# Kernel tuning notes

Hardware: AMD Instinct MI355X
Metric: run time of the kernel (lower is better)

## Reference

```python
import jax, jax.numpy as jnp
import numpy as np

D = 64          # data dimension
K = 16          # latent dimension
N = 65536       # number of samples
P = 2           # max_permutations
BETA = 10.0     # noise precision


def setup_inputs() -> dict:
    key = jax.random.key(0)
    kz, kw, ke, kp = jax.random.split(key, 4)
    W = jax.random.normal(kw, (D, K), jnp.float32)
    Z = jax.random.normal(kz, (N, K), jnp.float32)
    eps = (1.0 / BETA) * jax.random.normal(ke, (N, 1), jnp.float32)
    x = Z @ W.T + eps  # (N, D), matches the repo's generative model
    # one permutation of 0..D-1 per (dim a, permutation p)
    keys = jax.random.split(kp, D * P)
    perms = jax.vmap(lambda k: jax.random.permutation(k, D))(keys)
    perms = perms.reshape(D, P, D).astype(jnp.int32)
    return {"x": x, "W": W, "perms": perms}


def _masked_loss(x, W, perms):
    n = x.shape[0]
    log2pi = jnp.asarray(np.log(2.0 * np.pi), x.dtype)
    noise_eye = jnp.eye(D, dtype=x.dtype) / BETA
    total = jnp.zeros((), x.dtype)
    for a in range(D):
        m = a + 1
        loss_pred = jnp.zeros((n,), x.dtype)
        for p in range(P):
            perm = perms[a, p]
            Wp = W[perm]            # (D, K)
            xp = x[:, perm]         # (N, D)
            S = Wp @ Wp.T + noise_eye  # (D, D)
            if m == D:
                m_pred = jnp.zeros_like(xp)       # no conditioning set left
                v_pred = jnp.diagonal(S)          # (D,)
            else:
                S_mr = S[:m, m:]                              # (m, r)
                iS_rr = jnp.linalg.inv(S[m:, m:])             # (r, r)
                A = S_mr @ iS_rr                              # (m, r)
                m_pred = xp[:, m:] @ A.T                      # (N, m)
                v_pred = jnp.diagonal(S[:m, :m] - A @ S_mr.T) # (m,)
            diff = xp[:, :m] - m_pred
            log_p = -0.5 * jnp.log(v_pred) - 0.5 * log2pi - 0.5 * diff * diff / v_pred
            loss_pred = loss_pred + log_p.sum(axis=1)
        total = total + loss_pred.sum() / (P * m * n)
    return -total


def reference(x, W, perms):
    return _masked_loss(x, W, perms)
```

## Files before the change

kernel.cpp:

```cpp
#include <hip/hip_runtime.h>
#include <math.h>

#define D 64
#define K 16
#define PP 2
#define NN 65536
#define LOG2PI 1.8378770664093454
#define NOISE 0.1
#define NPAIR (D * PP)

#define RCHUNK 128
#define NCH (NN / RCHUNK)

__device__ float  g_part[NCH * D * D];
__device__ float  g_Gf[D * D];
__device__ double g_Ud[NPAIR * K * D];
__device__ double g_dvd[NPAIR * D];

__global__ __launch_bounds__(256) void gram_prep_kernel(const float* __restrict__ x,
                                                        const float* __restrict__ W,
                                                        const int* __restrict__ perms,
                                                        float* __restrict__ out) {
    const int tid = threadIdx.x;
    const int wave = tid >> 6;
    const int lane = tid & 63;

    if (blockIdx.x < NCH) {
        if (blockIdx.x == 0 && tid == 0) out[0] = 0.0f;
        __shared__ float xs[RCHUNK * D];
        const int i0 = (lane >> 3) << 3;
        const int j0 = (lane & 7) << 3;
        float acc[8][8];
#pragma unroll
        for (int u = 0; u < 8; ++u)
#pragma unroll
            for (int v = 0; v < 8; ++v) acc[u][v] = 0.0f;

        {
            const int cb = blockIdx.x;
            const float4* src = (const float4*)(x + (size_t)cb * RCHUNK * D);
            float4* dst = (float4*)xs;
#pragma unroll
            for (int u = 0; u < 8; ++u)
                dst[tid + 256 * u] = src[tid + 256 * u];
            __syncthreads();
            const float4* xr = (const float4*)xs;
#pragma unroll 2
            for (int rr = 0; rr < 32; ++rr) {
                const int r = (wave << 5) + rr;
                const float4 a0 = xr[(r << 4) + (i0 >> 2)];
                const float4 a1 = xr[(r << 4) + (i0 >> 2) + 1];
                const float4 b0 = xr[(r << 4) + (j0 >> 2)];
                const float4 b1 = xr[(r << 4) + (j0 >> 2) + 1];
                const float av[8] = {a0.x, a0.y, a0.z, a0.w, a1.x, a1.y, a1.z, a1.w};
                const float bv[8] = {b0.x, b0.y, b0.z, b0.w, b1.x, b1.y, b1.z, b1.w};
#pragma unroll
                for (int u = 0; u < 8; ++u)
#pragma unroll
                    for (int v = 0; v < 8; ++v)
                        acc[u][v] = fmaf(av[u], bv[v], acc[u][v]);
            }
            __syncthreads();
        }
        float* red = xs;
        if (wave < 2) {
            float* base = red + (wave << 12);
#pragma unroll
            for (int u = 0; u < 8; ++u) {
                float4 w0 = {acc[u][0], acc[u][1], acc[u][2], acc[u][3]};
                float4 w1 = {acc[u][4], acc[u][5], acc[u][6], acc[u][7]};
                *(float4*)&base[(i0 + u) * D + j0] = w0;
                *(float4*)&base[(i0 + u) * D + j0 + 4] = w1;
            }
        }
        __syncthreads();
        if (wave >= 2) {
            float* base = red + ((wave - 2) << 12);
#pragma unroll
            for (int u = 0; u < 8; ++u) {
                float4 w0 = *(const float4*)&base[(i0 + u) * D + j0];
                float4 w1 = *(const float4*)&base[(i0 + u) * D + j0 + 4];
                w0.x += acc[u][0]; w0.y += acc[u][1]; w0.z += acc[u][2]; w0.w += acc[u][3];
                w1.x += acc[u][4]; w1.y += acc[u][5]; w1.z += acc[u][6]; w1.w += acc[u][7];
                *(float4*)&base[(i0 + u) * D + j0] = w0;
                *(float4*)&base[(i0 + u) * D + j0 + 4] = w1;
            }
        }
        __syncthreads();
        float* p = g_part + (size_t)blockIdx.x * (D * D);
        for (int e = tid; e < D * D; e += 256)
            p[e] = red[e] + red[4096 + e];
        return;
    }

    const int pair = blockIdx.x - NCH;
    const int m = pair / PP + 1;

    __shared__ int perm[D];
    __shared__ float Wp[D][K + 1];
    __shared__ float Wz[D][K];
    __shared__ double Mlds[K][K + 1];
    __shared__ double Minv[K][K + 1];
    __shared__ double dvp[4][D];

    if (tid < D) perm[tid] = perms[pair * D + tid];
    __syncthreads();
    for (int e = tid; e < D * K; e += 256) {
        int i = e >> 4, k = e & (K - 1);
        float w = W[perm[i] * K + k];
        Wp[i][k] = w;
        Wz[i][k] = (i >= m) ? w : 0.0f;
    }
    __syncthreads();

    {
        const int k1 = tid >> 4, k2 = tid & 15;
        double s = (k1 == k2) ? NOISE : 0.0;
#pragma unroll
        for (int sr = 0; sr < D; ++sr)
            s += (double)Wz[sr][k1] * (double)Wz[sr][k2];
        Mlds[k1][k2] = s;
    }
    __syncthreads();

    if (wave == 0) {
        const int r = lane & 15;
        const int ch = lane >> 4;
        double a[8];
#pragma unroll
        for (int j = 0; j < 8; ++j) {
            if (ch < 2) a[j] = Mlds[r][ch * 8 + j];
            else a[j] = ((ch - 2) * 8 + j == r) ? 1.0 : 0.0;
        }
        for (int k = 0; k < K; ++k) {
            const int chk = k >> 3;
            const int rk = k & 7;
            double colk = a[rk];
            double fme = __shfl(colk, (chk << 4) | r, 64);
            double piv = __shfl(colk, (chk << 4) | k, 64);
            double pinv = 1.0 / piv;
            double p[8];
#pragma unroll
            for (int j = 0; j < 8; ++j)
                p[j] = __shfl(a[j], (ch << 4) | k, 64) * pinv;
            if (r == k) {
#pragma unroll
                for (int j = 0; j < 8; ++j) a[j] = p[j];
            } else {
#pragma unroll
                for (int j = 0; j < 8; ++j) a[j] -= fme * p[j];
            }
        }
        if (ch >= 2)
#pragma unroll
            for (int j = 0; j < 8; ++j) Minv[r][(ch - 2) * 8 + j] = a[j];
    }
    __syncthreads();

    {
        const int j = tid & 63;
        const int kb = tid >> 6;
        double* Up = g_Ud + (size_t)pair * (K * D);
        double pdv = 0.0;
#pragma unroll
        for (int u = 0; u < 4; ++u) {
            const int k = kb + 4 * u;
            double s = 0.0;
#pragma unroll
            for (int k2 = 0; k2 < K; ++k2)
                s += Minv[k][k2] * (double)Wp[j][k2];
            Up[k * D + j] = s;
            pdv += (double)Wp[j][k] * s;
        }
        dvp[kb][j] = pdv;
    }
    __syncthreads();
    if (tid < D)
        g_dvd[(size_t)pair * D + tid] = dvp[0][tid] + dvp[1][tid] + dvp[2][tid] + dvp[3][tid];
}

__global__ __launch_bounds__(256) void reduce_kernel() {
    const int tid = threadIdx.x;
    const int le = tid >> 4;
    const int sub = tid & 15;
    const int e = blockIdx.x * 16 + le;
    __shared__ double ps[16][17];
    double s0 = 0.0, s1 = 0.0;
    for (int b = sub; b < NCH; b += 32)
        s0 += (double)g_part[(size_t)b * (D * D) + e];
    for (int b = sub + 16; b < NCH; b += 32)
        s1 += (double)g_part[(size_t)b * (D * D) + e];
    ps[le][sub] = s0 + s1;
    __syncthreads();
    if (sub == 0) {
        double t = 0.0;
#pragma unroll
        for (int i = 0; i < 16; ++i) t += ps[le][i];
        g_Gf[e] = (float)t;
    }
}

__global__ __launch_bounds__(256) void pair2_kernel(const float* __restrict__ W,
                                                    const int* __restrict__ perms,
                                                    float* __restrict__ out) {
    const int pair = blockIdx.x;
    const int m = pair / PP + 1;
    const int tid = threadIdx.x;

    __shared__ int perm[D];
    __shared__ float Wz[D][K];
    __shared__ float Gp[D][D + 1];
    __shared__ double Y[K][D + 1];
    __shared__ double Z[K][K + 1];
    __shared__ double Ush[K][D + 1];
    __shared__ double qp[4][D];

    double dvv = 0.0;
    if (tid < D) dvv = g_dvd[(size_t)pair * D + tid];

    if (tid < D) perm[tid] = perms[pair * D + tid];
    __syncthreads();
    for (int e = tid; e < D * K; e += 256) {
        int i = e >> 4, k = e & (K - 1);
        float w = W[perm[i] * K + k];
        Wz[i][k] = (i >= m) ? w : 0.0f;
    }
    for (int e = tid; e < D * D; e += 256) {
        int i = e >> 6, t = e & 63;
        Gp[i][t] = g_Gf[perm[i] * D + perm[t]];
    }
    for (int e = tid; e < K * D; e += 256)
        Ush[e >> 6][e & 63] = g_Ud[(size_t)pair * (K * D) + e];
    __syncthreads();

    {
        const int j = tid & 63;
        const int kb = tid >> 6;
        double s0 = 0.0, s1 = 0.0, s2 = 0.0, s3 = 0.0;
#pragma unroll
        for (int sr = 0; sr < D; ++sr) {
            const float4 wv = *(const float4*)&Wz[sr][4 * kb];
            const double g = (double)Gp[sr][j];
            s0 += (double)wv.x * g;
            s1 += (double)wv.y * g;
            s2 += (double)wv.z * g;
            s3 += (double)wv.w * g;
        }
        Y[4 * kb][j] = s0;
        Y[4 * kb + 1][j] = s1;
        Y[4 * kb + 2][j] = s2;
        Y[4 * kb + 3][j] = s3;
    }
    __syncthreads();

    {
        const int k1 = tid >> 4, k2 = tid & 15;
        double s = 0.0;
#pragma unroll
        for (int sr = 0; sr < D; ++sr)
            s += Y[k1][sr] * (double)Wz[sr][k2];
        Z[k1][k2] = s;
    }
    __syncthreads();

    {
        const int lane4 = tid & 3;
        const int j = tid >> 2;
        double t1 = 0.0, t2 = 0.0;
#pragma unroll
        for (int k1 = lane4; k1 < K; k1 += 4) {
            const double uj = Ush[k1][j];
            t1 += uj * Y[k1][j];
            double zs = 0.0;
#pragma unroll
            for (int k2 = 0; k2 < K; ++k2) zs += Z[k1][k2] * Ush[k2][j];
            t2 += uj * zs;
        }
        qp[lane4][j] = -2.0 * t1 + t2;
    }
    __syncthreads();

    if (tid < D) {
        const int j = tid;
        double tj = 0.0;
        if (j < m) {
            const double v = NOISE * (1.0 + dvv);
            const double q =
                (double)Gp[j][j] + qp[0][j] + qp[1][j] + qp[2][j] + qp[3][j];
            tj = -0.5 * log(v) - 0.5 * LOG2PI - 0.5 * q / (v * (double)NN);
        }
#pragma unroll
        for (int off = 32; off > 0; off >>= 1) tj += __shfl_down(tj, off, 64);
        if (tid == 0) atomicAdd(out, (float)(-tj / (double)(PP * m)));
    }
}

extern "C" void kernel_launch(void* const* d_in, const int* in_sizes, int n_in,
                              void* d_out, int out_size, void* d_ws, size_t ws_size,
                              hipStream_t stream) {
    const float* x = (const float*)d_in[0];
    const float* W = (const float*)d_in[1];
    const int* perms = (const int*)d_in[2];
    (void)d_ws; (void)ws_size;

    gram_prep_kernel<<<NCH + NPAIR, 256, 0, stream>>>(x, W, perms, (float*)d_out);
    reduce_kernel<<<256, 256, 0, stream>>>();
    pair2_kernel<<<NPAIR, 256, 0, stream>>>(W, perms, (float*)d_out);
}
```

Baseline: 98.59 us.

## Fuse gram, prep, reduce and pair stages into one persistent kernel with atomic counters

Merges the three launches into a single 512-block kernel. Every block computes one Gram chunk, then subsets of blocks do the per-pair precompute, the cross-chunk reduction, or the final pair evaluation, with ordering enforced by agent-scope atomic counters and spin-waits. The goal is to remove kernel launch gaps and let the pair precompute overlap with the Gram work. The cost is spin-waiting that assumes all 512 blocks can be co-resident (launch_bounds 256,2 with about 41 KB of LDS), plus counter resets at the end of each call.

```diff
diff --git a/kernel.cpp b/kernel.cpp
--- a/kernel.cpp
+++ b/kernel.cpp
@@ -11,23 +11,32 @@
 
 #define RCHUNK 128
 #define NCH (NN / RCHUNK)
+#define NRED 256
+#define SCOPE_AGENT __HIP_MEMORY_SCOPE_AGENT
 
 __device__ float  g_part[NCH * D * D];
 __device__ float  g_Gf[D * D];
 __device__ double g_Ud[NPAIR * K * D];
 __device__ double g_dvd[NPAIR * D];
-
-__global__ __launch_bounds__(256) void gram_prep_kernel(const float* __restrict__ x,
-                                                        const float* __restrict__ W,
-                                                        const int* __restrict__ perms,
-                                                        float* __restrict__ out) {
+__device__ int g_ctr_gram;
+__device__ int g_ctr_prep;
+__device__ int g_ctr_red;
+__device__ int g_ctr_done;
+
+__global__ __launch_bounds__(256, 2) void fused_kernel(const float* __restrict__ x,
+                                                       const float* __restrict__ W,
+                                                       const int* __restrict__ perms,
+                                                       float* __restrict__ out) {
+    const int bid = blockIdx.x;
     const int tid = threadIdx.x;
     const int wave = tid >> 6;
     const int lane = tid & 63;
-
-    if (blockIdx.x < NCH) {
-        if (blockIdx.x == 0 && tid == 0) out[0] = 0.0f;
-        __shared__ float xs[RCHUNK * D];
+    __shared__ __align__(16) char smem_raw[41856];
+
+    if (bid == 0 && tid == 0) out[0] = 0.0f;
+
+    {
+        float* xs = (float*)smem_raw;
         const int i0 = (lane >> 3) << 3;
         const int j0 = (lane & 7) << 3;
         float acc[8][8];
@@ -36,32 +45,29 @@
 #pragma unroll
             for (int v = 0; v < 8; ++v) acc[u][v] = 0.0f;
 
-        {
-            const int cb = blockIdx.x;
-            const float4* src = (const float4*)(x + (size_t)cb * RCHUNK * D);
-            float4* dst = (float4*)xs;
+        const float4* src = (const float4*)(x + (size_t)bid * RCHUNK * D);
+        float4* dst = (float4*)xs;
+#pragma unroll
+        for (int u = 0; u < 8; ++u)
+            dst[tid + 256 * u] = src[tid + 256 * u];
+        __syncthreads();
+        const float4* xr = (const float4*)xs;
+#pragma unroll 2
+        for (int rr = 0; rr < 32; ++rr) {
+            const int r = (wave << 5) + rr;
+            const float4 a0 = xr[(r << 4) + (i0 >> 2)];
+            const float4 a1 = xr[(r << 4) + (i0 >> 2) + 1];
+            const float4 b0 = xr[(r << 4) + (j0 >> 2)];
+            const float4 b1 = xr[(r << 4) + (j0 >> 2) + 1];
+            const float av[8] = {a0.x, a0.y, a0.z, a0.w, a1.x, a1.y, a1.z, a1.w};
+            const float bv[8] = {b0.x, b0.y, b0.z, b0.w, b1.x, b1.y, b1.z, b1.w};
 #pragma unroll
             for (int u = 0; u < 8; ++u)
-                dst[tid + 256 * u] = src[tid + 256 * u];
-            __syncthreads();
-            const float4* xr = (const float4*)xs;
-#pragma unroll 2
-            for (int rr = 0; rr < 32; ++rr) {
-                const int r = (wave << 5) + rr;
-                const float4 a0 = xr[(r << 4) + (i0 >> 2)];
-                const float4 a1 = xr[(r << 4) + (i0 >> 2) + 1];
-                const float4 b0 = xr[(r << 4) + (j0 >> 2)];
-                const float4 b1 = xr[(r << 4) + (j0 >> 2) + 1];
-                const float av[8] = {a0.x, a0.y, a0.z, a0.w, a1.x, a1.y, a1.z, a1.w};
-                const float bv[8] = {b0.x, b0.y, b0.z, b0.w, b1.x, b1.y, b1.z, b1.w};
-#pragma unroll
-                for (int u = 0; u < 8; ++u)
-#pragma unroll
-                    for (int v = 0; v < 8; ++v)
-                        acc[u][v] = fmaf(av[u], bv[v], acc[u][v]);
-            }
-            __syncthreads();
-        }
+#pragma unroll
+                for (int v = 0; v < 8; ++v)
+                    acc[u][v] = fmaf(av[u], bv[v], acc[u][v]);
+        }
+        __syncthreads();
         float* red = xs;
         if (wave < 2) {
             float* base = red + (wave << 12);
@@ -87,211 +93,248 @@
             }
         }
         __syncthreads();
-        float* p = g_part + (size_t)blockIdx.x * (D * D);
+        float* p = g_part + (size_t)bid * (D * D);
         for (int e = tid; e < D * D; e += 256)
             p[e] = red[e] + red[4096 + e];
+    }
+    __syncthreads();
+    if (tid == 0) {
+        __threadfence();
+        __hip_atomic_fetch_add(&g_ctr_gram, 1, __ATOMIC_RELEASE, SCOPE_AGENT);
+    }
+
+    if (bid < NPAIR) {
+        const int pair = bid;
+        const int m = pair / PP + 1;
+        double* Mlds = (double*)smem_raw;
+        double* Minv = (double*)(smem_raw + 2176);
+        double* dvp  = (double*)(smem_raw + 4352);
+        float*  Wp   = (float*)(smem_raw + 6400);
+        float*  Wz   = (float*)(smem_raw + 10752);
+        int*    perm = (int*)(smem_raw + 14848);
+
+        if (tid < D) perm[tid] = perms[pair * D + tid];
+        __syncthreads();
+        for (int e = tid; e < D * K; e += 256) {
+            int i = e >> 4, k = e & (K - 1);
+            float w = W[perm[i] * K + k];
+            Wp[i * 17 + k] = w;
+            Wz[i * 16 + k] = (i >= m) ? w : 0.0f;
+        }
+        __syncthreads();
+
+        {
+            const int k1 = tid >> 4, k2 = tid & 15;
+            double s = (k1 == k2) ? NOISE : 0.0;
+#pragma unroll
+            for (int sr = 0; sr < D; ++sr)
+                s += (double)Wz[sr * 16 + k1] * (double)Wz[sr * 16 + k2];
+            Mlds[k1 * 17 + k2] = s;
+        }
+        __syncthreads();
+
+        if (wave == 0) {
+            const int r = lane & 15;
+            const int ch = lane >> 4;
+            double a[8];
+#pragma unroll
+            for (int j = 0; j < 8; ++j) {
+                if (ch < 2) a[j] = Mlds[r * 17 + ch * 8 + j];
+                else a[j] = ((ch - 2) * 8 + j == r) ? 1.0 : 0.0;
+            }
+            for (int k = 0; k < K; ++k) {
+                const int chk = k >> 3;
+                const int rk = k & 7;
+                double colk = a[rk];
+                double fme = __shfl(colk, (chk << 4) | r, 64);
+                double piv = __shfl(colk, (chk << 4) | k, 64);
+                double pinv = 1.0 / piv;
+                double p[8];
+#pragma unroll
+                for (int j = 0; j < 8; ++j)
+                    p[j] = __shfl(a[j], (ch << 4) | k, 64) * pinv;
+                if (r == k) {
+#pragma unroll
+                    for (int j = 0; j < 8; ++j) a[j] = p[j];
+                } else {
+#pragma unroll
+                    for (int j = 0; j < 8; ++j) a[j] -= fme * p[j];
+                }
+            }
+            if (ch >= 2)
+#pragma unroll
+                for (int j = 0; j < 8; ++j) Minv[r * 17 + (ch - 2) * 8 + j] = a[j];
+        }
+        __syncthreads();
+
+        {
+            const int j = tid & 63;
+            const int kb = tid >> 6;
+            double* Up = g_Ud + (size_t)pair * (K * D);
+            double pdv = 0.0;
+#pragma unroll
+            for (int u = 0; u < 4; ++u) {
+                const int k = kb + 4 * u;
+                double s = 0.0;
+#pragma unroll
+                for (int k2 = 0; k2 < K; ++k2)
+                    s += Minv[k * 17 + k2] * (double)Wp[j * 17 + k2];
+                Up[k * D + j] = s;
+                pdv += (double)Wp[j * 17 + k] * s;
+            }
+            dvp[kb * 64 + j] = pdv;
+        }
+        __syncthreads();
+        if (tid < D)
+            g_dvd[(size_t)pair * D + tid] =
+                dvp[0 * 64 + tid] + dvp[1 * 64 + tid] + dvp[2 * 64 + tid] + dvp[3 * 64 + tid];
+        __syncthreads();
+        if (tid == 0) {
+            __threadfence();
+            __hip_atomic_fetch_add(&g_ctr_prep, 1, __ATOMIC_RELEASE, SCOPE_AGENT);
+        }
         return;
     }
 
-    const int pair = blockIdx.x - NCH;
-    const int m = pair / PP + 1;
-
-    __shared__ int perm[D];
-    __shared__ float Wp[D][K + 1];
-    __shared__ float Wz[D][K];
-    __shared__ double Mlds[K][K + 1];
-    __shared__ double Minv[K][K + 1];
-    __shared__ double dvp[4][D];
-
-    if (tid < D) perm[tid] = perms[pair * D + tid];
+    if (bid < NPAIR + NRED) {
+        if (tid == 0) {
+            while (__hip_atomic_load(&g_ctr_gram, __ATOMIC_ACQUIRE, SCOPE_AGENT) < NCH)
+                __builtin_amdgcn_s_sleep(4);
+        }
+        __syncthreads();
+        const int rb = bid - NPAIR;
+        double* ps = (double*)smem_raw;
+        const int le = tid >> 4;
+        const int sub = tid & 15;
+        const int e = rb * 16 + le;
+        double s0 = 0.0, s1 = 0.0;
+        for (int b = sub; b < NCH; b += 32)
+            s0 += (double)g_part[(size_t)b * (D * D) + e];
+        for (int b = sub + 16; b < NCH; b += 32)
+            s1 += (double)g_part[(size_t)b * (D * D) + e];
+        ps[le * 17 + sub] = s0 + s1;
+        __syncthreads();
+        if (sub == 0) {
+            double t = 0.0;
+#pragma unroll
+            for (int i = 0; i < 16; ++i) t += ps[le * 17 + i];
+            g_Gf[e] = (float)t;
+        }
+        __syncthreads();
+        if (tid == 0) {
+            __threadfence();
+            __hip_atomic_fetch_add(&g_ctr_red, 1, __ATOMIC_RELEASE, SCOPE_AGENT);
+        }
+        return;
+    }
+
+    if (tid == 0) {
+        while (__hip_atomic_load(&g_ctr_red, __ATOMIC_ACQUIRE, SCOPE_AGENT) < NRED)
+            __builtin_amdgcn_s_sleep(4);
+        while (__hip_atomic_load(&g_ctr_prep, __ATOMIC_ACQUIRE, SCOPE_AGENT) < NPAIR)
+            __builtin_amdgcn_s_sleep(4);
+    }
     __syncthreads();
-    for (int e = tid; e < D * K; e += 256) {
-        int i = e >> 4, k = e & (K - 1);
-        float w = W[perm[i] * K + k];
-        Wp[i][k] = w;
-        Wz[i][k] = (i >= m) ? w : 0.0f;
+    {
+        const int pair = bid - (NPAIR + NRED);
+        const int m = pair / PP + 1;
+        double* Y    = (double*)smem_raw;
+        double* Z    = (double*)(smem_raw + 8320);
+        double* Ush  = (double*)(smem_raw + 10496);
+        double* qp   = (double*)(smem_raw + 18816);
+        float*  Gp   = (float*)(smem_raw + 20864);
+        float*  Wz   = (float*)(smem_raw + 37504);
+        int*    perm = (int*)(smem_raw + 41600);
+
+        double dvv = 0.0;
+        if (tid < D) dvv = g_dvd[(size_t)pair * D + tid];
+
+        if (tid < D) perm[tid] = perms[pair * D + tid];
+        __syncthreads();
+        for (int e = tid; e < D * K; e += 256) {
+            int i = e >> 4, k = e & (K - 1);
+            float w = W[perm[i] * K + k];
+            Wz[i * 16 + k] = (i >= m) ? w : 0.0f;
+        }
+        for (int e = tid; e < D * D; e += 256) {
+            int i = e >> 6, t = e & 63;
+            Gp[i * 65 + t] = g_Gf[perm[i] * D + perm[t]];
+        }
+        for (int e = tid; e < K * D; e += 256)
+            Ush[(e >> 6) * 65 + (e & 63)] = g_Ud[(size_t)pair * (K * D) + e];
+        __syncthreads();
+
+        {
+            const int j = tid & 63;
+            const int kb = tid >> 6;
+            double s0 = 0.0, s1 = 0.0, s2 = 0.0, s3 = 0.0;
+#pragma unroll
+            for (int sr = 0; sr < D; ++sr) {
+                const float4 wv = *(const float4*)&Wz[sr * 16 + 4 * kb];
+                const double g = (double)Gp[sr * 65 + j];
+                s0 += (double)wv.x * g;
+                s1 += (double)wv.y * g;
+                s2 += (double)wv.z * g;
+                s3 += (double)wv.w * g;
+            }
+            Y[(4 * kb) * 65 + j] = s0;
+            Y[(4 * kb + 1) * 65 + j] = s1;
+            Y[(4 * kb + 2) * 65 + j] = s2;
+            Y[(4 * kb + 3) * 65 + j] = s3;
+        }
+        __syncthreads();
+
+        {
+            const int k1 = tid >> 4, k2 = tid & 15;
+            double s = 0.0;
+#pragma unroll
+            for (int sr = 0; sr < D; ++sr)
+                s += Y[k1 * 65 + sr] * (double)Wz[sr * 16 + k2];
+            Z[k1 * 17 + k2] = s;
+        }
+        __syncthreads();
+
+        {
+            const int lane4 = tid & 3;
+            const int j = tid >> 2;
+            double t1 = 0.0, t2 = 0.0;
+#pragma unroll
+            for (int k1 = lane4; k1 < K; k1 += 4) {
+                const double uj = Ush[k1 * 65 + j];
+                t1 += uj * Y[k1 * 65 + j];
+                double zs = 0.0;
+#pragma unroll
+                for (int k2 = 0; k2 < K; ++k2) zs += Z[k1 * 17 + k2] * Ush[k2 * 65 + j];
+                t2 += uj * zs;
+            }
+            qp[lane4 * 64 + j] = -2.0 * t1 + t2;
+        }
+        __syncthreads();
+
+        if (tid < D) {
+            const int j = tid;
+            double tj = 0.0;
+            if (j < m) {
+                const double v = NOISE * (1.0 + dvv);
+                const double q = (double)Gp[j * 65 + j] +
+                                 qp[0 * 64 + j] + qp[1 * 64 + j] + qp[2 * 64 + j] + qp[3 * 64 + j];
+                tj = -0.5 * log(v) - 0.5 * LOG2PI - 0.5 * q / (v * (double)NN);
+            }
+#pragma unroll
+            for (int off = 32; off > 0; off >>= 1) tj += __shfl_down(tj, off, 64);
+            if (tid == 0) atomicAdd(out, (float)(-tj / (double)(PP * m)));
+        }
     }
     __syncthreads();
-
-    {
-        const int k1 = tid >> 4, k2 = tid & 15;
-        double s = (k1 == k2) ? NOISE : 0.0;
-#pragma unroll
-        for (int sr = 0; sr < D; ++sr)
-            s += (double)Wz[sr][k1] * (double)Wz[sr][k2];
-        Mlds[k1][k2] = s;
-    }
-    __syncthreads();
-
-    if (wave == 0) {
-        const int r = lane & 15;
-        const int ch = lane >> 4;
-        double a[8];
-#pragma unroll
-        for (int j = 0; j < 8; ++j) {
-            if (ch < 2) a[j] = Mlds[r][ch * 8 + j];
-            else a[j] = ((ch - 2) * 8 + j == r) ? 1.0 : 0.0;
-        }
-        for (int k = 0; k < K; ++k) {
-            const int chk = k >> 3;
-            const int rk = k & 7;
-            double colk = a[rk];
-            double fme = __shfl(colk, (chk << 4) | r, 64);
-            double piv = __shfl(colk, (chk << 4) | k, 64);
-            double pinv = 1.0 / piv;
-            double p[8];
-#pragma unroll
-            for (int j = 0; j < 8; ++j)
-                p[j] = __shfl(a[j], (ch << 4) | k, 64) * pinv;
-            if (r == k) {
-#pragma unroll
-                for (int j = 0; j < 8; ++j) a[j] = p[j];
-            } else {
-#pragma unroll
-                for (int j = 0; j < 8; ++j) a[j] -= fme * p[j];
-            }
-        }
-        if (ch >= 2)
-#pragma unroll
-            for (int j = 0; j < 8; ++j) Minv[r][(ch - 2) * 8 + j] = a[j];
-    }
-    __syncthreads();
-
-    {
-        const int j = tid & 63;
-        const int kb = tid >> 6;
-        double* Up = g_Ud + (size_t)pair * (K * D);
-        double pdv = 0.0;
-#pragma unroll
-        for (int u = 0; u < 4; ++u) {
-            const int k = kb + 4 * u;
-            double s = 0.0;
-#pragma unroll
-            for (int k2 = 0; k2 < K; ++k2)
-                s += Minv[k][k2] * (double)Wp[j][k2];
-            Up[k * D + j] = s;
-            pdv += (double)Wp[j][k] * s;
-        }
-        dvp[kb][j] = pdv;
-    }
-    __syncthreads();
-    if (tid < D)
-        g_dvd[(size_t)pair * D + tid] = dvp[0][tid] + dvp[1][tid] + dvp[2][tid] + dvp[3][tid];
-}
-
-__global__ __launch_bounds__(256) void reduce_kernel() {
-    const int tid = threadIdx.x;
-    const int le = tid >> 4;
-    const int sub = tid & 15;
-    const int e = blockIdx.x * 16 + le;
-    __shared__ double ps[16][17];
-    double s0 = 0.0, s1 = 0.0;
-    for (int b = sub; b < NCH; b += 32)
-        s0 += (double)g_part[(size_t)b * (D * D) + e];
-    for (int b = sub + 16; b < NCH; b += 32)
-        s1 += (double)g_part[(size_t)b * (D * D) + e];
-    ps[le][sub] = s0 + s1;
-    __syncthreads();
-    if (sub == 0) {
-        double t = 0.0;
-#pragma unroll
-        for (int i = 0; i < 16; ++i) t += ps[le][i];
-        g_Gf[e] = (float)t;
-    }
-}
-
-__global__ __launch_bounds__(256) void pair2_kernel(const float* __restrict__ W,
-                                                    const int* __restrict__ perms,
-                                                    float* __restrict__ out) {
-    const int pair = blockIdx.x;
-    const int m = pair / PP + 1;
-    const int tid = threadIdx.x;
-
-    __shared__ int perm[D];
-    __shared__ float Wz[D][K];
-    __shared__ float Gp[D][D + 1];
-    __shared__ double Y[K][D + 1];
-    __shared__ double Z[K][K + 1];
-    __shared__ double Ush[K][D + 1];
-    __shared__ double qp[4][D];
-
-    double dvv = 0.0;
-    if (tid < D) dvv = g_dvd[(size_t)pair * D + tid];
-
-    if (tid < D) perm[tid] = perms[pair * D + tid];
-    __syncthreads();
-    for (int e = tid; e < D * K; e += 256) {
-        int i = e >> 4, k = e & (K - 1);
-        float w = W[perm[i] * K + k];
-        Wz[i][k] = (i >= m) ? w : 0.0f;
-    }
-    for (int e = tid; e < D * D; e += 256) {
-        int i = e >> 6, t = e & 63;
-        Gp[i][t] = g_Gf[perm[i] * D + perm[t]];
-    }
-    for (int e = tid; e < K * D; e += 256)
-        Ush[e >> 6][e & 63] = g_Ud[(size_t)pair * (K * D) + e];
-    __syncthreads();
-
-    {
-        const int j = tid & 63;
-        const int kb = tid >> 6;
-        double s0 = 0.0, s1 = 0.0, s2 = 0.0, s3 = 0.0;
-#pragma unroll
-        for (int sr = 0; sr < D; ++sr) {
-            const float4 wv = *(const float4*)&Wz[sr][4 * kb];
-            const double g = (double)Gp[sr][j];
-            s0 += (double)wv.x * g;
-            s1 += (double)wv.y * g;
-            s2 += (double)wv.z * g;
-            s3 += (double)wv.w * g;
-        }
-        Y[4 * kb][j] = s0;
-        Y[4 * kb + 1][j] = s1;
-        Y[4 * kb + 2][j] = s2;
-        Y[4 * kb + 3][j] = s3;
-    }
-    __syncthreads();
-
-    {
-        const int k1 = tid >> 4, k2 = tid & 15;
-        double s = 0.0;
-#pragma unroll
-        for (int sr = 0; sr < D; ++sr)
-            s += Y[k1][sr] * (double)Wz[sr][k2];
-        Z[k1][k2] = s;
-    }
-    __syncthreads();
-
-    {
-        const int lane4 = tid & 3;
-        const int j = tid >> 2;
-        double t1 = 0.0, t2 = 0.0;
-#pragma unroll
-        for (int k1 = lane4; k1 < K; k1 += 4) {
-            const double uj = Ush[k1][j];
-            t1 += uj * Y[k1][j];
-            double zs = 0.0;
-#pragma unroll
-            for (int k2 = 0; k2 < K; ++k2) zs += Z[k1][k2] * Ush[k2][j];
-            t2 += uj * zs;
-        }
-        qp[lane4][j] = -2.0 * t1 + t2;
-    }
-    __syncthreads();
-
-    if (tid < D) {
-        const int j = tid;
-        double tj = 0.0;
-        if (j < m) {
-            const double v = NOISE * (1.0 + dvv);
-            const double q =
-                (double)Gp[j][j] + qp[0][j] + qp[1][j] + qp[2][j] + qp[3][j];
-            tj = -0.5 * log(v) - 0.5 * LOG2PI - 0.5 * q / (v * (double)NN);
-        }
-#pragma unroll
-        for (int off = 32; off > 0; off >>= 1) tj += __shfl_down(tj, off, 64);
-        if (tid == 0) atomicAdd(out, (float)(-tj / (double)(PP * m)));
+    if (tid == 0) {
+        __threadfence();
+        int old = __hip_atomic_fetch_add(&g_ctr_done, 1, __ATOMIC_ACQ_REL, SCOPE_AGENT);
+        if (old == NPAIR - 1) {
+            __hip_atomic_store(&g_ctr_gram, 0, __ATOMIC_RELAXED, SCOPE_AGENT);
+            __hip_atomic_store(&g_ctr_prep, 0, __ATOMIC_RELAXED, SCOPE_AGENT);
+            __hip_atomic_store(&g_ctr_red, 0, __ATOMIC_RELAXED, SCOPE_AGENT);
+            __hip_atomic_store(&g_ctr_done, 0, __ATOMIC_RELAXED, SCOPE_AGENT);
+        }
     }
 }
 
@@ -303,7 +346,5 @@
     const int* perms = (const int*)d_in[2];
     (void)d_ws; (void)ws_size;
 
-    gram_prep_kernel<<<NCH + NPAIR, 256, 0, stream>>>(x, W, perms, (float*)d_out);
-    reduce_kernel<<<256, 256, 0, stream>>>();
-    pair2_kernel<<<NPAIR, 256, 0, stream>>>(W, perms, (float*)d_out);
+    fused_kernel<<<NCH, 256, 0, stream>>>(x, W, perms, (float*)d_out);
 }
```

Result: slower. 204.8 us (+107.7%).
